# Performance work log

Hardware: AMD Instinct MI355X
Metric: run time of the kernel (lower is better)

## Reference

```python
import jax, jax.numpy as jnp
import numpy as np

N_NODES = 50000
N_EDGES = 800000
C_IN = 128
HEADS = 4
C_HEAD = 32  # c_out // heads = 128 // 4
NEG_SLOPE = 0.2


def setup_inputs() -> dict:
    key = jax.random.key(0)
    k_x, k_e, k_w, k_as, k_ad, k_b = jax.random.split(key, 6)
    x = jax.random.normal(k_x, (N_NODES, C_IN), dtype=jnp.float32)
    edge_index = jax.random.randint(k_e, (2, N_EDGES), 0, N_NODES, dtype=jnp.int64)
    # xavier_uniform_ with gain=1.414 on lin.weight [H*C, C_IN] -> same bound for W [C_IN, H*C]
    bound = 1.414 * np.sqrt(6.0 / (C_IN + HEADS * C_HEAD))
    W = jax.random.uniform(k_w, (C_IN, HEADS * C_HEAD), minval=-bound, maxval=bound, dtype=jnp.float32)
    # glorot init for attention vectors (PyG default)
    ab = np.sqrt(6.0 / (1 + HEADS * C_HEAD))
    att_src = jax.random.uniform(k_as, (HEADS, C_HEAD), minval=-ab, maxval=ab, dtype=jnp.float32)
    att_dst = jax.random.uniform(k_ad, (HEADS, C_HEAD), minval=-ab, maxval=ab, dtype=jnp.float32)
    bias = jnp.zeros((HEADS * C_HEAD,), dtype=jnp.float32)
    return {"x": x, "edge_index": edge_index, "W": W,
            "att_src": att_src, "att_dst": att_dst, "bias": bias}


def reference(x, edge_index, W, att_src, att_dst, bias):
    N = x.shape[0]
    H, C = att_src.shape
    # Linear projection, per-head split: [N, H, C]
    xl = (x @ W).reshape(N, H, C)
    a_src = jnp.einsum('nhc,hc->nh', xl, att_src)  # [N, H]
    a_dst = jnp.einsum('nhc,hc->nh', xl, att_dst)  # [N, H]

    src, dst = edge_index[0], edge_index[1]
    loop = jnp.arange(N, dtype=edge_index.dtype)
    # GATConv(add_self_loops=True): remove existing self loops, then add one per node.
    src_f = jnp.concatenate([src, loop])  # [E+N]
    dst_f = jnp.concatenate([dst, loop])
    drop = jnp.concatenate([src == dst, jnp.zeros((N,), dtype=bool)])

    e = jax.nn.leaky_relu(a_src[src_f] + a_dst[dst_f], NEG_SLOPE)  # [E+N, H]
    e = jnp.where(drop[:, None], -jnp.inf, e)

    # segment softmax over edges sharing a destination (every node has a self loop -> max is finite)
    m = jax.ops.segment_max(e, dst_f, num_segments=N)          # [N, H]
    ex = jnp.exp(e - m[dst_f])                                  # [E+N, H]
    denom = jax.ops.segment_sum(ex, dst_f, num_segments=N)     # [N, H]
    alpha = ex / denom[dst_f]                                   # [E+N, H]

    msg = xl[src_f] * alpha[:, :, None]                         # [E+N, H, C]
    out = jax.ops.segment_sum(msg, dst_f, num_segments=N)      # [N, H, C]
    out = out.reshape(N, H * C) + bias
    return out / jnp.sqrt(jnp.asarray(H, dtype=out.dtype))
```

## Files before the change

kernel.cpp:

```cpp
#include <hip/hip_runtime.h>
#include <math.h>

#define CDIM 128
#define HEADS 4
#define NEG 0.2f
#define BSTRIDE 64

typedef __attribute__((ext_vector_type(8))) short bf16x8;
typedef __attribute__((ext_vector_type(8))) unsigned short u16x8;
typedef __attribute__((ext_vector_type(4))) float f32x4;

static __device__ __forceinline__ unsigned short f2bf(float f) {
    unsigned u = __float_as_uint(f);
    u += 0x7FFFu + ((u >> 16) & 1u);
    return (unsigned short)(u >> 16);
}
static __device__ __forceinline__ float bf2f(unsigned short s) {
    return __uint_as_float((unsigned)s << 16);
}

#define LDS_STRIDE 136

__global__ __launch_bounds__(256) void wt_kernel(const float* __restrict__ W,
                                                 unsigned short* __restrict__ WT,
                                                 int* __restrict__ counts, int nClr) {
    int f = blockIdx.x * 256 + threadIdx.x;
    for (int i = f; i < nClr; i += 4096) counts[i] = 0;
    int k = f >> 5, c4 = (f & 31) * 4;
    float4 v = *(const float4*)(W + (size_t)k * CDIM + c4);
    WT[(size_t)(c4 + 0) * CDIM + k] = f2bf(v.x);
    WT[(size_t)(c4 + 1) * CDIM + k] = f2bf(v.y);
    WT[(size_t)(c4 + 2) * CDIM + k] = f2bf(v.z);
    WT[(size_t)(c4 + 3) * CDIM + k] = f2bf(v.w);
}

__global__ __launch_bounds__(256) void gemm_hist_kernel(const float* __restrict__ x,
                                                        const unsigned short* __restrict__ WT,
                                                        const float* __restrict__ att_src,
                                                        const float* __restrict__ att_dst,
                                                        unsigned short* __restrict__ xlh,
                                                        float* __restrict__ a_src,
                                                        float* __restrict__ a_dst, int N,
                                                        const int* __restrict__ esrc,
                                                        const int* __restrict__ edst,
                                                        int* __restrict__ counts,
                                                        unsigned* __restrict__ packed, int E,
                                                        int gemmBlocks) {
    __shared__ unsigned short As[64 * LDS_STRIDE];

    if ((int)blockIdx.x >= gemmBlocks) {
        int e = (blockIdx.x - gemmBlocks) * 256 + threadIdx.x;
        if (e < E) {
            int s = esrc[e], d = edst[e];
            unsigned pk = ~0u;
            if (s != d) {
                int r = atomicAdd(&counts[d], 1);
                pk = (unsigned)d | ((unsigned)r << 16);
            }
            packed[e] = pk;
        }
        return;
    }

    const int tid = threadIdx.x;
    const int row0 = blockIdx.x * 64;

#pragma unroll
    for (int i = 0; i < 8; ++i) {
        int f = tid + i * 256;
        int r = f >> 5, k4 = f & 31;
        float4 v = make_float4(0.f, 0.f, 0.f, 0.f);
        int gr = row0 + r;
        if (gr < N) v = *(const float4*)(x + (size_t)gr * CDIM + k4 * 4);
        ushort4 h;
        h.x = f2bf(v.x); h.y = f2bf(v.y); h.z = f2bf(v.z); h.w = f2bf(v.w);
        *(ushort4*)(&As[r * LDS_STRIDE + k4 * 4]) = h;
    }
    __syncthreads();

    const int wave = tid >> 6;
    const int lane = tid & 63;
    const int m    = lane & 15;
    const int quad = lane >> 4;
    const int wrow = wave * 16;

    bf16x8 a[4];
#pragma unroll
    for (int ks = 0; ks < 4; ++ks)
        a[ks] = *(const bf16x8*)(&As[(wrow + m) * LDS_STRIDE + ks * 32 + quad * 8]);

    f32x4 acc[8];
#pragma unroll
    for (int t = 0; t < 8; ++t) {
        f32x4 c = {0.f, 0.f, 0.f, 0.f};
#pragma unroll
        for (int ks = 0; ks < 4; ++ks) {
            bf16x8 b = *(const bf16x8*)(WT + (size_t)(t * 16 + m) * CDIM + ks * 32 + quad * 8);
            c = __builtin_amdgcn_mfma_f32_16x16x32_bf16(a[ks], b, c, 0, 0, 0);
        }
        acc[t] = c;
    }

    __syncthreads();
#pragma unroll
    for (int t = 0; t < 8; ++t)
#pragma unroll
        for (int reg = 0; reg < 4; ++reg)
            As[(wrow + quad * 4 + reg) * LDS_STRIDE + t * 16 + m] = f2bf(acc[t][reg]);
    __syncthreads();
    {
        int r = tid >> 2;
        int c = (tid & 3) * 32;
        int grow = row0 + r;
        if (grow < N) {
            u16x8 v0 = *(const u16x8*)(&As[r * LDS_STRIDE + c]);
            u16x8 v1 = *(const u16x8*)(&As[r * LDS_STRIDE + c + 8]);
            u16x8 v2 = *(const u16x8*)(&As[r * LDS_STRIDE + c + 16]);
            u16x8 v3 = *(const u16x8*)(&As[r * LDS_STRIDE + c + 24]);
            *(u16x8*)(xlh + (size_t)grow * CDIM + c)      = v0;
            *(u16x8*)(xlh + (size_t)grow * CDIM + c + 8)  = v1;
            *(u16x8*)(xlh + (size_t)grow * CDIM + c + 16) = v2;
            *(u16x8*)(xlh + (size_t)grow * CDIM + c + 24) = v3;
        }
    }

    float ps[4][4], pd[4][4];
#pragma unroll
    for (int h = 0; h < 4; ++h)
#pragma unroll
        for (int reg = 0; reg < 4; ++reg) { ps[h][reg] = 0.f; pd[h][reg] = 0.f; }
#pragma unroll
    for (int t = 0; t < 8; ++t) {
        int h = t >> 1;
        float vs = att_src[t * 16 + m];
        float vd = att_dst[t * 16 + m];
#pragma unroll
        for (int reg = 0; reg < 4; ++reg) {
            ps[h][reg] += acc[t][reg] * vs;
            pd[h][reg] += acc[t][reg] * vd;
        }
    }
#pragma unroll
    for (int off = 8; off > 0; off >>= 1) {
#pragma unroll
        for (int h = 0; h < 4; ++h)
#pragma unroll
            for (int reg = 0; reg < 4; ++reg) {
                ps[h][reg] += __shfl_down(ps[h][reg], off, 16);
                pd[h][reg] += __shfl_down(pd[h][reg], off, 16);
            }
    }
    if (m == 0) {
#pragma unroll
        for (int reg = 0; reg < 4; ++reg) {
            int row = row0 + wrow + quad * 4 + reg;
            if (row < N) {
#pragma unroll
                for (int h = 0; h < 4; ++h) {
                    a_src[row * 4 + h] = ps[h][reg];
                    a_dst[row * 4 + h] = pd[h][reg];
                }
            }
        }
    }
}

__global__ __launch_bounds__(256) void scatter_kernel(const int* __restrict__ src,
                                                      const unsigned* __restrict__ packed,
                                                      int* __restrict__ bucket, int E) {
    int base = (blockIdx.x * 256 + threadIdx.x) * 2;
    if (base + 2 <= E) {
        int2 s2 = *(const int2*)(src + base);
        uint2 p2 = *(const uint2*)(packed + base);
        unsigned r0 = p2.x >> 16, r1 = p2.y >> 16;
        if (p2.x != ~0u && r0 < BSTRIDE) bucket[(p2.x & 0xFFFFu) * BSTRIDE + r0] = s2.x;
        if (p2.y != ~0u && r1 < BSTRIDE) bucket[(p2.y & 0xFFFFu) * BSTRIDE + r1] = s2.y;
    } else if (base < E) {
        unsigned pk = packed[base];
        unsigned r = pk >> 16;
        if (pk != ~0u && r < BSTRIDE) bucket[(pk & 0xFFFFu) * BSTRIDE + r] = src[base];
    }
}

__global__ __launch_bounds__(256) void gather_kernel(const int* __restrict__ counts,
                                                     const int* __restrict__ bucket,
                                                     const unsigned short* __restrict__ xlh,
                                                     const float* __restrict__ a_src,
                                                     const float* __restrict__ a_dst,
                                                     const float* __restrict__ bias,
                                                     float* __restrict__ out, int N) {
    const int node = blockIdx.x * 4 + (threadIdx.x >> 6);
    const int lane = threadIdx.x & 63;
    const int g = lane >> 4;
    const int lane16 = lane & 15;
    if (node >= N) return;
    const int c8 = lane16 * 8;
    const int h = lane16 >> 2;

    const float ad = a_dst[node * 4 + h];
    const int beg = node * BSTRIDE;
    int cnt = counts[node];
    if (cnt > BSTRIDE) cnt = BSTRIDE;

    float acc[8];
#pragma unroll
    for (int i = 0; i < 8; ++i) acc[i] = 0.f;
    float den = 0.f;

    int j = g;
    for (; j + 12 < cnt; j += 16) {
        int s[4];
#pragma unroll
        for (int q = 0; q < 4; ++q) s[q] = bucket[beg + j + 4 * q];
        float e[4];
#pragma unroll
        for (int q = 0; q < 4; ++q) e[q] = a_src[s[q] * 4 + h] + ad;
        u16x8 u[4];
#pragma unroll
        for (int q = 0; q < 4; ++q) u[q] = *(const u16x8*)(xlh + (size_t)s[q] * CDIM + c8);
        float w[4];
#pragma unroll
        for (int q = 0; q < 4; ++q) {
            float eq = e[q] > 0.f ? e[q] : NEG * e[q];
            w[q] = __expf(eq);
        }
#pragma unroll
        for (int q = 0; q < 4; ++q) {
#pragma unroll
            for (int i = 0; i < 8; ++i) acc[i] += w[q] * bf2f(u[q][i]);
            den += w[q];
        }
    }
    for (; j < cnt; j += 4) {
        int s = bucket[beg + j];
        float e = a_src[s * 4 + h] + ad;
        u16x8 u = *(const u16x8*)(xlh + (size_t)s * CDIM + c8);
        e = e > 0.f ? e : NEG * e;
        float w = __expf(e);
#pragma unroll
        for (int i = 0; i < 8; ++i) acc[i] += w * bf2f(u[i]);
        den += w;
    }
    if (g == 0) {
        float es = a_src[node * 4 + h] + ad;
        es = es > 0.f ? es : NEG * es;
        float ws = __expf(es);
        u16x8 u = *(const u16x8*)(xlh + (size_t)node * CDIM + c8);
#pragma unroll
        for (int i = 0; i < 8; ++i) acc[i] += ws * bf2f(u[i]);
        den += ws;
    }
#pragma unroll
    for (int i = 0; i < 8; ++i) {
        acc[i] += __shfl_xor(acc[i], 16);
        acc[i] += __shfl_xor(acc[i], 32);
    }
    den += __shfl_xor(den, 16);
    den += __shfl_xor(den, 32);

    if (g == 0) {
        float inv = 1.0f / den;
        float4 b0 = *(const float4*)(bias + c8);
        float4 b1 = *(const float4*)(bias + c8 + 4);
        float4 o0, o1;
        o0.x = (acc[0] * inv + b0.x) * 0.5f;
        o0.y = (acc[1] * inv + b0.y) * 0.5f;
        o0.z = (acc[2] * inv + b0.z) * 0.5f;
        o0.w = (acc[3] * inv + b0.w) * 0.5f;
        o1.x = (acc[4] * inv + b1.x) * 0.5f;
        o1.y = (acc[5] * inv + b1.y) * 0.5f;
        o1.z = (acc[6] * inv + b1.z) * 0.5f;
        o1.w = (acc[7] * inv + b1.w) * 0.5f;
        *(float4*)(out + (size_t)node * CDIM + c8) = o0;
        *(float4*)(out + (size_t)node * CDIM + c8 + 4) = o1;
    }
}

extern "C" void kernel_launch(void* const* d_in, const int* in_sizes, int n_in,
                              void* d_out, int out_size, void* d_ws, size_t ws_size,
                              hipStream_t stream) {
    const float* x       = (const float*)d_in[0];
    const int*   ei      = (const int*)d_in[1];
    const float* W       = (const float*)d_in[2];
    const float* att_src = (const float*)d_in[3];
    const float* att_dst = (const float*)d_in[4];
    const float* bias    = (const float*)d_in[5];
    float* out = (float*)d_out;

    const int N = in_sizes[0] / CDIM;
    const int E = in_sizes[1] / 2;

    char* wsb = (char*)d_ws;
    unsigned short* xlh = (unsigned short*)wsb;         wsb += (size_t)N * CDIM * sizeof(unsigned short);
    unsigned short* WT  = (unsigned short*)wsb;         wsb += (size_t)CDIM * CDIM * sizeof(unsigned short);
    float* a_src = (float*)wsb;                         wsb += (size_t)N * HEADS * sizeof(float);
    float* a_dst = (float*)wsb;                         wsb += (size_t)N * HEADS * sizeof(float);
    int* counts  = (int*)wsb;                           wsb += (size_t)N * sizeof(int);
    unsigned* packed = (unsigned*)wsb;                  wsb += (size_t)E * sizeof(unsigned);
    int* bucket  = (int*)wsb;                           wsb += (size_t)N * BSTRIDE * sizeof(int);

    wt_kernel<<<16, 256, 0, stream>>>(W, WT, counts, N);
    const int gemmBlocks = (N + 63) / 64;
    const int histBlocks = (E + 255) / 256;
    gemm_hist_kernel<<<gemmBlocks + histBlocks, 256, 0, stream>>>(
        x, WT, att_src, att_dst, xlh, a_src, a_dst, N, ei, ei + E, counts, packed, E, gemmBlocks);
    scatter_kernel<<<((E + 1) / 2 + 255) / 256, 256, 0, stream>>>(ei, packed, bucket, E);
    gather_kernel<<<(N + 3) / 4, 256, 0, stream>>>(counts, bucket, xlh, a_src, a_dst, bias, out, N);
}
```

Measured before the change: 174.8 us.

## Replace per-node atomic bucketing with two-pass superbucket binning via LDS

Edges are first binned by groups of 64 destination nodes into superbuckets using one atomic per group, storing source and local destination packed together. A second kernel loads each superbucket, distributes its entries into per-node slots with shared-memory atomics, and writes counts and the bucket tile contiguously. This is meant to replace the scattered global atomics and random bucket writes with more local, coalesced traffic. The trade-offs are heavier atomic contention on fewer counters and a fixed superbucket capacity that drops edges if a group exceeds it. Packing the source into 16 bits also limits node ids to below 65536.

```diff
diff --git a/kernel.cpp b/kernel.cpp
--- a/kernel.cpp
+++ b/kernel.cpp
@@ -5,6 +5,7 @@
 #define HEADS 4
 #define NEG 0.2f
 #define BSTRIDE 64
+#define SCAP 1536
 
 typedef __attribute__((ext_vector_type(8))) short bf16x8;
 typedef __attribute__((ext_vector_type(8))) unsigned short u16x8;
@@ -23,9 +24,9 @@
 
 __global__ __launch_bounds__(256) void wt_kernel(const float* __restrict__ W,
                                                  unsigned short* __restrict__ WT,
-                                                 int* __restrict__ counts, int nClr) {
+                                                 int* __restrict__ super_cnt, int nsb) {
     int f = blockIdx.x * 256 + threadIdx.x;
-    for (int i = f; i < nClr; i += 4096) counts[i] = 0;
+    for (int i = f; i < nsb; i += 4096) super_cnt[i] = 0;
     int k = f >> 5, c4 = (f & 31) * 4;
     float4 v = *(const float4*)(W + (size_t)k * CDIM + c4);
     WT[(size_t)(c4 + 0) * CDIM + k] = f2bf(v.x);
@@ -34,30 +35,30 @@
     WT[(size_t)(c4 + 3) * CDIM + k] = f2bf(v.w);
 }
 
-__global__ __launch_bounds__(256) void gemm_hist_kernel(const float* __restrict__ x,
-                                                        const unsigned short* __restrict__ WT,
-                                                        const float* __restrict__ att_src,
-                                                        const float* __restrict__ att_dst,
-                                                        unsigned short* __restrict__ xlh,
-                                                        float* __restrict__ a_src,
-                                                        float* __restrict__ a_dst, int N,
-                                                        const int* __restrict__ esrc,
-                                                        const int* __restrict__ edst,
-                                                        int* __restrict__ counts,
-                                                        unsigned* __restrict__ packed, int E,
-                                                        int gemmBlocks) {
+__global__ __launch_bounds__(256) void gemm_passA_kernel(const float* __restrict__ x,
+                                                         const unsigned short* __restrict__ WT,
+                                                         const float* __restrict__ att_src,
+                                                         const float* __restrict__ att_dst,
+                                                         unsigned short* __restrict__ xlh,
+                                                         float* __restrict__ a_src,
+                                                         float* __restrict__ a_dst, int N,
+                                                         const int* __restrict__ esrc,
+                                                         const int* __restrict__ edst,
+                                                         int* __restrict__ super_cnt,
+                                                         unsigned* __restrict__ super_bucket,
+                                                         int E, int gemmBlocks) {
     __shared__ unsigned short As[64 * LDS_STRIDE];
 
     if ((int)blockIdx.x >= gemmBlocks) {
         int e = (blockIdx.x - gemmBlocks) * 256 + threadIdx.x;
         if (e < E) {
             int s = esrc[e], d = edst[e];
-            unsigned pk = ~0u;
             if (s != d) {
-                int r = atomicAdd(&counts[d], 1);
-                pk = (unsigned)d | ((unsigned)r << 16);
+                int p = d >> 6;
+                int r = atomicAdd(&super_cnt[p], 1);
+                if (r < SCAP)
+                    super_bucket[(size_t)p * SCAP + r] = (unsigned)s | ((unsigned)(d & 63) << 16);
             }
-            packed[e] = pk;
         }
         return;
     }
@@ -165,21 +166,31 @@
     }
 }
 
-__global__ __launch_bounds__(256) void scatter_kernel(const int* __restrict__ src,
-                                                      const unsigned* __restrict__ packed,
-                                                      int* __restrict__ bucket, int E) {
-    int base = (blockIdx.x * 256 + threadIdx.x) * 2;
-    if (base + 2 <= E) {
-        int2 s2 = *(const int2*)(src + base);
-        uint2 p2 = *(const uint2*)(packed + base);
-        unsigned r0 = p2.x >> 16, r1 = p2.y >> 16;
-        if (p2.x != ~0u && r0 < BSTRIDE) bucket[(p2.x & 0xFFFFu) * BSTRIDE + r0] = s2.x;
-        if (p2.y != ~0u && r1 < BSTRIDE) bucket[(p2.y & 0xFFFFu) * BSTRIDE + r1] = s2.y;
-    } else if (base < E) {
-        unsigned pk = packed[base];
-        unsigned r = pk >> 16;
-        if (pk != ~0u && r < BSTRIDE) bucket[(pk & 0xFFFFu) * BSTRIDE + r] = src[base];
-    }
+__global__ __launch_bounds__(256) void passB_kernel(const int* __restrict__ super_cnt,
+                                                    const unsigned* __restrict__ super_bucket,
+                                                    int* __restrict__ counts,
+                                                    int* __restrict__ bucket, int N) {
+    __shared__ int lcnt[64];
+    __shared__ unsigned tile[64 * BSTRIDE];
+    const int p = blockIdx.x;
+    const int tid = threadIdx.x;
+    if (tid < 64) lcnt[tid] = 0;
+    __syncthreads();
+
+    int cnt = super_cnt[p];
+    if (cnt > SCAP) cnt = SCAP;
+    for (int i = tid; i < cnt; i += 256) {
+        unsigned en = super_bucket[(size_t)p * SCAP + i];
+        int dl = en >> 16;
+        int r = atomicAdd(&lcnt[dl], 1);
+        if (r < BSTRIDE) tile[dl * BSTRIDE + r] = en & 0xFFFFu;
+    }
+    __syncthreads();
+
+    int node0 = p * 64;
+    if (tid < 64 && node0 + tid < N) counts[node0 + tid] = lcnt[tid];
+    for (int i = tid; i < 64 * BSTRIDE; i += 256)
+        bucket[(size_t)p * 64 * BSTRIDE + i] = (int)tile[i];
 }
 
 __global__ __launch_bounds__(256) void gather_kernel(const int* __restrict__ counts,
@@ -289,6 +300,7 @@
 
     const int N = in_sizes[0] / CDIM;
     const int E = in_sizes[1] / 2;
+    const int NSB = (N + 63) >> 6;
 
     char* wsb = (char*)d_ws;
     unsigned short* xlh = (unsigned short*)wsb;         wsb += (size_t)N * CDIM * sizeof(unsigned short);
@@ -296,14 +308,15 @@
     float* a_src = (float*)wsb;                         wsb += (size_t)N * HEADS * sizeof(float);
     float* a_dst = (float*)wsb;                         wsb += (size_t)N * HEADS * sizeof(float);
     int* counts  = (int*)wsb;                           wsb += (size_t)N * sizeof(int);
-    unsigned* packed = (unsigned*)wsb;                  wsb += (size_t)E * sizeof(unsigned);
-    int* bucket  = (int*)wsb;                           wsb += (size_t)N * BSTRIDE * sizeof(int);
-
-    wt_kernel<<<16, 256, 0, stream>>>(W, WT, counts, N);
+    int* super_cnt = (int*)wsb;                         wsb += (size_t)NSB * sizeof(int);
+    unsigned* super_bucket = (unsigned*)wsb;            wsb += (size_t)NSB * SCAP * sizeof(unsigned);
+    int* bucket  = (int*)wsb;                           wsb += (size_t)NSB * 64 * BSTRIDE * sizeof(int);
+
+    wt_kernel<<<16, 256, 0, stream>>>(W, WT, super_cnt, NSB);
     const int gemmBlocks = (N + 63) / 64;
     const int histBlocks = (E + 255) / 256;
-    gemm_hist_kernel<<<gemmBlocks + histBlocks, 256, 0, stream>>>(
-        x, WT, att_src, att_dst, xlh, a_src, a_dst, N, ei, ei + E, counts, packed, E, gemmBlocks);
-    scatter_kernel<<<((E + 1) / 2 + 255) / 256, 256, 0, stream>>>(ei, packed, bucket, E);
+    gemm_passA_kernel<<<gemmBlocks + histBlocks, 256, 0, stream>>>(
+        x, WT, att_src, att_dst, xlh, a_src, a_dst, N, ei, ei + E, super_cnt, super_bucket, E, gemmBlocks);
+    passB_kernel<<<NSB, 256, 0, stream>>>(super_cnt, super_bucket, counts, bucket, N);
     gather_kernel<<<(N + 3) / 4, 256, 0, stream>>>(counts, bucket, xlh, a_src, a_dst, bias, out, N);
 }
```

New measurement: 320.3 us. +83.2%, slower.
